# Kernel optimization log

Hardware: AMD Instinct MI355X
Metric: run time of the kernel (lower is better)

Reference implementation:

```python
import jax, jax.numpy as jnp
import numpy as np

B, S, T, E, H, F = 2, 2048, 2048, 1024, 16, 4096
HD = E // H
EPS = 1e-5


def setup_inputs() -> dict:
    key = jax.random.key(0)
    ks = jax.random.split(key, 16)
    def w(k, shape):
        return (jax.random.normal(k, shape, jnp.float32) * 0.02)
    d = {
        "x": jax.random.normal(ks[0], (B, S, E), jnp.float32),
        "enc": jax.random.normal(ks[1], (B, T, E), jnp.float32),
    }
    for i, n in enumerate(["sa_q", "sa_k", "sa_v", "sa_o", "ca_q", "ca_k", "ca_v", "ca_o"]):
        d[n + "w"] = w(ks[2 + i], (E, E))  # torch Linear: [out, in]
        d[n + "b"] = jnp.zeros((E,), jnp.float32)
    d["w1"] = w(ks[10], (F, E)); d["b1"] = jnp.zeros((F,), jnp.float32)
    d["w2"] = w(ks[11], (E, F)); d["b2"] = jnp.zeros((E,), jnp.float32)
    for n in ["ln1", "ln2", "ln3"]:
        d[n + "_g"] = jnp.ones((E,), jnp.float32)
        d[n + "_b"] = jnp.zeros((E,), jnp.float32)
    return d


def _layernorm(x, g, b):
    m = jnp.mean(x, axis=-1, keepdims=True)
    v = jnp.mean((x - m) ** 2, axis=-1, keepdims=True)
    return (x - m) / jnp.sqrt(v + EPS) * g + b


def _heads(x, w, b):
    bsz, sl, _ = x.shape
    y = x @ w.T + b
    return y.reshape(bsz, sl, H, HD).transpose(0, 2, 1, 3)  # [B,H,S,hd]


def _mha(xq, xkv, qw, qb, kw, kb, vw, vb, ow, ob, causal):
    q = _heads(xq, qw, qb)
    k = _heads(xkv, kw, kb)
    v = _heads(xkv, vw, vb)
    scores = jnp.einsum('bhsd,bhtd->bhst', q, k) / np.sqrt(HD).astype(np.float32)
    if causal:
        sl, tl = scores.shape[-2], scores.shape[-1]
        mask = jnp.tril(jnp.ones((sl, tl), bool))
        scores = jnp.where(mask, scores, -jnp.inf)
    a = jax.nn.softmax(scores, axis=-1)
    o = jnp.einsum('bhst,bhtd->bhsd', a, v)
    o = o.transpose(0, 2, 1, 3).reshape(xq.shape[0], xq.shape[1], E)
    return o @ ow.T + ob


def reference(x, enc,
              sa_qw, sa_qb, sa_kw, sa_kb, sa_vw, sa_vb, sa_ow, sa_ob,
              ca_qw, ca_qb, ca_kw, ca_kb, ca_vw, ca_vb, ca_ow, ca_ob,
              w1, b1, w2, b2,
              ln1_g, ln1_b, ln2_g, ln2_b, ln3_g, ln3_b):
    sa = _mha(x, x, sa_qw, sa_qb, sa_kw, sa_kb, sa_vw, sa_vb, sa_ow, sa_ob, True)
    x = _layernorm(x + sa, ln1_g, ln1_b)
    ca = _mha(x, enc, ca_qw, ca_qb, ca_kw, ca_kb, ca_vw, ca_vb, ca_ow, ca_ob, False)
    x = _layernorm(x + ca, ln2_g, ln2_b)
    ffn = jax.nn.relu(x @ w1.T + b1) @ w2.T + b2
    return _layernorm(x + ffn, ln3_g, ln3_b)
```

## Files before the change

kernel.cpp:

```cpp
#include <hip/hip_runtime.h>
#include <hip/hip_bf16.h>
#include <stdint.h>

typedef __attribute__((ext_vector_type(8))) short s16x8;
typedef __attribute__((ext_vector_type(4))) short s16x4;
typedef __attribute__((ext_vector_type(4))) float f32x4;

#define DEV static __device__ __forceinline__

DEV ushort f2bu(float f){
  unsigned u = __builtin_bit_cast(unsigned, f);
  return (ushort)((u + 0x7fffu + ((u >> 16) & 1u)) >> 16);
}
DEV ushort f2bn(float f){
  return __builtin_bit_cast(ushort, __float2bfloat16(f));
}

DEV void gload16(const void* g, void* l){
  __builtin_amdgcn_global_load_lds((const __attribute__((address_space(1))) void*)g,
                                   (__attribute__((address_space(3))) void*)l, 16, 0, 0);
}

#define SCALE_C 0.18033688f

struct ConvArgs {
  const float* src[17];
  void*        dst[17];
  int blk_end[17];
  int nel[17];
  unsigned f32mask;
};

__global__ void __launch_bounds__(256) k_conv(ConvArgs a){
  int bi = blockIdx.x, seg = 0;
  while (bi >= a.blk_end[seg]) seg++;
  int b0 = seg ? a.blk_end[seg-1] : 0;
  long off = (long)(bi - b0)*2048 + (long)threadIdx.x*8;
  if (off >= a.nel[seg]) return;
  const float* s = a.src[seg] + off;
  f32x4 v0 = *(const f32x4*)s;
  f32x4 v1 = *(const f32x4*)(s+4);
  if ((a.f32mask >> seg) & 1u){
    float* d = (float*)a.dst[seg] + off;
    *(f32x4*)d = v0; *(f32x4*)(d+4) = v1;
  } else {
    ushort* d = (ushort*)a.dst[seg] + off;
    s16x8 o;
#pragma unroll
    for (int j = 0; j < 4; j++){ o[j] = (short)f2bu(v0[j]); o[4+j] = (short)f2bu(v1[j]); }
    *(s16x8*)d = o;
  }
}

__global__ void __launch_bounds__(256) k_gemm(const ushort* __restrict__ A, const ushort* __restrict__ W,
    const float* __restrict__ bias, ushort* __restrict__ Cb,
    int M, int N, int K, int lda, int ldb, float scale)
{
  __shared__ __align__(16) ushort lsA[2][128*64];
  __shared__ __align__(16) ushort lsB[2][128*64];
  const int t = threadIdx.x, w = t >> 6, u = t & 63, lr = u & 15, lk = u >> 4;
  const int m0 = blockIdx.y * 128, n0 = blockIdx.x * 128;
  const int wm = w >> 1, wn = w & 1;
  const int rA = t >> 3, c8 = (t & 7) * 8;
  const ushort* Ap = A + (size_t)(m0 + rA) * lda + c8;
  const ushort* Wp = W + (size_t)(n0 + rA) * ldb + c8;
  f32x4 acc[4][4] = {};
  const int nk = K >> 6;

  auto stage = [&](int k0, int buf){
#pragma unroll
    for (int j = 0; j < 4; j++){
      gload16(Ap + (size_t)j*32*lda + k0, &lsA[buf][0] + j*2048 + w*512);
      gload16(Wp + (size_t)j*32*ldb + k0, &lsB[buf][0] + j*2048 + w*512);
    }
  };
  stage(0, 0);
  for (int tk = 0; tk < nk; ++tk){
    __syncthreads();
    if (tk + 1 < nk) stage((tk + 1) << 6, (tk + 1) & 1);
    const ushort* La = &lsA[tk & 1][0];
    const ushort* Lb = &lsB[tk & 1][0];
#pragma unroll
    for (int ks = 0; ks < 2; ks++){
      s16x8 af[4], bfr[4];
#pragma unroll
      for (int i = 0; i < 4; i++) af[i]  = *(const s16x8*)(La + (wm*64 + i*16 + lr)*64 + ks*32 + lk*8);
#pragma unroll
      for (int i = 0; i < 4; i++) bfr[i] = *(const s16x8*)(Lb + (wn*64 + i*16 + lr)*64 + ks*32 + lk*8);
#pragma unroll
      for (int mi = 0; mi < 4; mi++)
#pragma unroll
        for (int ni = 0; ni < 4; ni++)
          acc[mi][ni] = __builtin_amdgcn_mfma_f32_16x16x32_bf16(af[mi], bfr[ni], acc[mi][ni], 0, 0, 0);
    }
  }

#pragma unroll
  for (int mi = 0; mi < 4; mi++){
#pragma unroll
    for (int ni = 0; ni < 4; ni++){
      const int row = m0 + wm*64 + mi*16 + lk*4;
      const int col = n0 + wn*64 + ni*16 + lr;
      const float bv = bias[col];
#pragma unroll
      for (int i = 0; i < 4; i++){
        float v = (acc[mi][ni][i] + bv) * scale;
        Cb[(size_t)(row + i) * N + col] = f2bn(v);
      }
    }
  }
}

__global__ void __launch_bounds__(256) k_gemmS(const ushort* __restrict__ A, const ushort* __restrict__ W,
    const float* __restrict__ bias, float* __restrict__ Cf,
    int M, int N, int Kext, int lda, int ldb, long long sstride)
{
  __shared__ __align__(16) ushort lsA[2][128*64];
  __shared__ __align__(16) ushort lsB[2][128*64];
  const int t = threadIdx.x, w = t >> 6, u = t & 63, lr = u & 15, lk = u >> 4;
  const int m0 = blockIdx.y * 128, n0 = blockIdx.x * 128;
  const int s = blockIdx.z;
  const int wm = w >> 1, wn = w & 1;
  const int rA = t >> 3, c8 = (t & 7) * 8;
  const ushort* Ap = A + (size_t)(m0 + rA) * lda + (size_t)s * Kext + c8;
  const ushort* Wp = W + (size_t)(n0 + rA) * ldb + (size_t)s * Kext + c8;
  if (s){ bias = nullptr; Cf += sstride; }
  f32x4 acc[4][4] = {};
  const int nk = Kext >> 6;

  auto stage = [&](int k0, int buf){
#pragma unroll
    for (int j = 0; j < 4; j++){
      gload16(Ap + (size_t)j*32*lda + k0, &lsA[buf][0] + j*2048 + w*512);
      gload16(Wp + (size_t)j*32*ldb + k0, &lsB[buf][0] + j*2048 + w*512);
    }
  };
  stage(0, 0);
  for (int tk = 0; tk < nk; ++tk){
    __syncthreads();
    if (tk + 1 < nk) stage((tk + 1) << 6, (tk + 1) & 1);
    const ushort* La = &lsA[tk & 1][0];
    const ushort* Lb = &lsB[tk & 1][0];
#pragma unroll
    for (int ks = 0; ks < 2; ks++){
      s16x8 af[4], bfr[4];
#pragma unroll
      for (int i = 0; i < 4; i++) af[i]  = *(const s16x8*)(La + (wm*64 + i*16 + lr)*64 + ks*32 + lk*8);
#pragma unroll
      for (int i = 0; i < 4; i++) bfr[i] = *(const s16x8*)(Lb + (wn*64 + i*16 + lr)*64 + ks*32 + lk*8);
#pragma unroll
      for (int mi = 0; mi < 4; mi++)
#pragma unroll
        for (int ni = 0; ni < 4; ni++)
          acc[mi][ni] = __builtin_amdgcn_mfma_f32_16x16x32_bf16(af[mi], bfr[ni], acc[mi][ni], 0, 0, 0);
    }
  }

#pragma unroll
  for (int mi = 0; mi < 4; mi++){
#pragma unroll
    for (int ni = 0; ni < 4; ni++){
      const int row = m0 + wm*64 + mi*16 + lk*4;
      const int col = n0 + wn*64 + ni*16 + lr;
      const float bv = bias ? bias[col] : 0.f;
#pragma unroll
      for (int i = 0; i < 4; i++)
        Cf[(size_t)(row + i) * N + col] = acc[mi][ni][i] + bv;
    }
  }
}

template<int MODE>
__global__ void __launch_bounds__(512, 1) k_gemm256(const ushort* __restrict__ A, const ushort* __restrict__ W,
    const float* __restrict__ bias, ushort* __restrict__ Cb,
    int N, int Ktot, int lda, int ldb, int scaleLim, float scale)
{
  __shared__ __align__(16) ushort lsA[2][256*64];
  __shared__ __align__(16) ushort lsB[2][256*64];
  const int t = threadIdx.x, w = t >> 6, u = t & 63, lr = u & 15, lk = u >> 4;
  const int gx = gridDim.x;
  const int nwg = gx * gridDim.y;
  const int id = blockIdx.y * gx + blockIdx.x;
  const int swz = (id & 7) * (nwg >> 3) + (id >> 3);
  const int n0 = (swz % gx) * 256, m0 = (swz / gx) * 256;
  const int wm = w >> 2, wn = w & 3;
  const int nt = Ktot >> 6;

  const int r0 = w*8 + (u >> 3), cc = u & 7;
  const int csw = 8 * (cc ^ (r0 & 7));
  const ushort* Ap = A + (size_t)(m0 + r0) * lda + csw;
  const ushort* Wp = W + (size_t)(n0 + r0) * ldb + csw;

  f32x4 acc[8][4] = {};
  const int swl = lr & 7;
  s16x8 afr[4], bfr[4];

#pragma unroll
  for (int j = 0; j < 4; j++){
    gload16(Ap + (size_t)(64*j)*lda, &lsA[0][0] + w*512 + j*4096);
    gload16(Wp + (size_t)(64*j)*ldb, &lsB[0][0] + w*512 + j*4096);
  }
  asm volatile("s_waitcnt vmcnt(0)" ::: "memory");
  __builtin_amdgcn_s_barrier();

  for (int tk = 0; tk < nt; ++tk){
    const char* La = (const char*)&lsA[tk & 1][0];
    const char* Lb = (const char*)&lsB[tk & 1][0];
    ushort* dA = &lsA[(tk & 1) ^ 1][0] + w*512;
    ushort* dB = &lsB[(tk & 1) ^ 1][0] + w*512;
    const bool pf = (tk + 1 < nt);
    const size_t k1 = (size_t)(tk + 1) << 6;

#pragma unroll
    for (int i = 0; i < 4; i++)
      afr[i] = *(const s16x8*)(La + (wm*128 + i*16 + lr)*128 + ((lk ^ swl) * 16));
#pragma unroll
    for (int i = 0; i < 4; i++)
      bfr[i] = *(const s16x8*)(Lb + (wn*64 + i*16 + lr)*128 + ((lk ^ swl) * 16));
    if (pf){
      gload16(Ap + k1, dA);
      gload16(Wp + k1, dB);
      gload16(Ap + (size_t)64*lda + k1, dA + 4096);
      gload16(Wp + (size_t)64*ldb + k1, dB + 4096);
    }
    __builtin_amdgcn_s_barrier();
    asm volatile("s_waitcnt lgkmcnt(0)" ::: "memory");
    __builtin_amdgcn_s_setprio(1);
#pragma unroll
    for (int mi = 0; mi < 4; mi++)
#pragma unroll
      for (int ni = 0; ni < 4; ni++)
        acc[mi][ni] = __builtin_amdgcn_mfma_f32_16x16x32_bf16(afr[mi], bfr[ni], acc[mi][ni], 0, 0, 0);
    __builtin_amdgcn_s_setprio(0);
    __builtin_amdgcn_s_barrier();

#pragma unroll
    for (int i = 0; i < 4; i++)
      afr[i] = *(const s16x8*)(La + (wm*128 + 64 + i*16 + lr)*128 + ((lk ^ swl) * 16));
    if (pf){
      gload16(Ap + (size_t)128*lda + k1, dA + 8192);
      gload16(Wp + (size_t)128*ldb + k1, dB + 8192);
      gload16(Ap + (size_t)192*lda + k1, dA + 12288);
      gload16(Wp + (size_t)192*ldb + k1, dB + 12288);
    }
    __builtin_amdgcn_s_barrier();
    asm volatile("s_waitcnt lgkmcnt(0)" ::: "memory");
    __builtin_amdgcn_s_setprio(1);
#pragma unroll
    for (int mi = 0; mi < 4; mi++)
#pragma unroll
      for (int ni = 0; ni < 4; ni++)
        acc[4+mi][ni] = __builtin_amdgcn_mfma_f32_16x16x32_bf16(afr[mi], bfr[ni], acc[4+mi][ni], 0, 0, 0);
    __builtin_amdgcn_s_setprio(0);
    __builtin_amdgcn_s_barrier();

#pragma unroll
    for (int i = 0; i < 4; i++)
      afr[i] = *(const s16x8*)(La + (wm*128 + i*16 + lr)*128 + (((4 + lk) ^ swl) * 16));
#pragma unroll
    for (int i = 0; i < 4; i++)
      bfr[i] = *(const s16x8*)(Lb + (wn*64 + i*16 + lr)*128 + (((4 + lk) ^ swl) * 16));
    __builtin_amdgcn_s_barrier();
    asm volatile("s_waitcnt lgkmcnt(0)" ::: "memory");
    __builtin_amdgcn_s_setprio(1);
#pragma unroll
    for (int mi = 0; mi < 4; mi++)
#pragma unroll
      for (int ni = 0; ni < 4; ni++)
        acc[mi][ni] = __builtin_amdgcn_mfma_f32_16x16x32_bf16(afr[mi], bfr[ni], acc[mi][ni], 0, 0, 0);
    __builtin_amdgcn_s_setprio(0);
    __builtin_amdgcn_s_barrier();

#pragma unroll
    for (int i = 0; i < 4; i++)
      afr[i] = *(const s16x8*)(La + (wm*128 + 64 + i*16 + lr)*128 + (((4 + lk) ^ swl) * 16));
    __builtin_amdgcn_s_barrier();
    asm volatile("s_waitcnt lgkmcnt(0)" ::: "memory");
    __builtin_amdgcn_s_setprio(1);
#pragma unroll
    for (int mi = 0; mi < 4; mi++)
#pragma unroll
      for (int ni = 0; ni < 4; ni++)
        acc[4+mi][ni] = __builtin_amdgcn_mfma_f32_16x16x32_bf16(afr[mi], bfr[ni], acc[4+mi][ni], 0, 0, 0);
    __builtin_amdgcn_s_setprio(0);
    asm volatile("s_waitcnt vmcnt(0)" ::: "memory");
    __builtin_amdgcn_s_barrier();
  }

#pragma unroll
  for (int mi = 0; mi < 8; mi++){
#pragma unroll
    for (int ni = 0; ni < 4; ni++){
      const int row = m0 + wm*128 + mi*16 + lk*4;
      const int col = n0 + wn*64 + ni*16 + lr;
      const float bv = bias[col];
#pragma unroll
      for (int i = 0; i < 4; i++){
        float v = acc[mi][ni][i] + bv;
        if (MODE == 2) v = fmaxf(v, 0.f);
        if (MODE == 0 && col < scaleLim) v *= scale;
        Cb[(size_t)(row + i) * N + col] = f2bn(v);
      }
    }
  }
}

__global__ void __launch_bounds__(256) k_vt(const ushort* __restrict__ V, ushort* __restrict__ Vt,
                                            int stride, int S)
{
  __shared__ ushort tile[64][72];
  const int st = blockIdx.x*64, h = blockIdx.y, b = blockIdx.z;
  const int r = threadIdx.x >> 3, c8 = (threadIdx.x & 7)*8;
#pragma unroll
  for (int j = 0; j < 2; j++){
    int s = r + j*32;
    s16x8 v = *(const s16x8*)(V + (size_t)(b*S + st + s)*stride + h*64 + c8);
    *(s16x8*)&tile[s][c8] = v;
  }
  __syncthreads();
#pragma unroll
  for (int j = 0; j < 2; j++){
    int d = r + j*32;
    s16x8 o;
#pragma unroll
    for (int e = 0; e < 8; e++) o[e] = tile[c8+e][d];
    *(s16x8*)(Vt + ((size_t)((b*16 + h)*64 + d))*S + st + c8) = o;
  }
}

template<bool CAUSAL>
__global__ void __launch_bounds__(512, 4) k_attn(const ushort* __restrict__ Q, const ushort* __restrict__ Kg,
    const ushort* __restrict__ Vt, ushort* __restrict__ O, int sQ, int sK, int SQ, int SKV)
{
  __shared__ __align__(16) ushort Kl[2][128*64];
  __shared__ __align__(16) ushort Vl[2][64*128];
  __shared__ __align__(16) ushort Pl[8][16*64];
  const int t = threadIdx.x, w = t >> 6, u = t & 63, lr = u & 15, lk = u >> 4;
  const int hb = blockIdx.x;
  const int b = hb >> 4, h = hb & 15;
  const int krow = t >> 3, kcol = t & 7;
  const int vrow = t >> 4, vcol = t & 15;
  const size_t kvbase = (size_t)b * SKV;
  const size_t vtbase = (size_t)((b*16 + h)*64);
  char* Pc = (char*)&Pl[w][0];
  const int swzq = (lr & 7) << 4;

  auto stage = [&](int kt, int buf){
#pragma unroll
    for (int p = 0; p < 2; p++){
      int row = krow + p*64;
      gload16(Kg + (kvbase + kt*128 + row)*sK + h*64 + 8*(kcol ^ (row & 7)),
              &Kl[buf][0] + t*8 + p*4096);
      int d = vrow + p*32;
      gload16(Vt + (vtbase + d)*SKV + kt*128 + 8*(vcol ^ (d & 7)),
              &Vl[buf][0] + t*8 + p*4096);
    }
  };

  const int NREP = CAUSAL ? 2 : 1;
#pragma unroll 1
  for (int rep = 0; rep < NREP; rep++){
    const int qt = CAUSAL ? (rep ? (int)blockIdx.y : (int)(2*gridDim.y - 1 - blockIdx.y))
                          : (int)blockIdx.y;
    const int q0 = qt * 128;

    const ushort* qp = Q + (size_t)(b*SQ + q0 + w*16 + lr) * sQ + h*64 + lk*8;
    s16x8 qf0 = *(const s16x8*)qp;
    s16x8 qf1 = *(const s16x8*)(qp + 32);

    f32x4 oacc[4] = {};
    f32x4 lacc = {};
    const int nkt = CAUSAL ? (qt + 1) : (SKV >> 7);

    stage(0, 0);
    __syncthreads();

    for (int kt = 0; kt < nkt; kt++){
      const int buf = kt & 1;
      if (kt + 1 < nkt) stage(kt + 1, buf ^ 1);
      char* Kc = (char*)&Kl[buf][0];
      char* Vc = (char*)&Vl[buf][0];

      f32x4 sacc[8] = {};
      __builtin_amdgcn_s_setprio(1);
#pragma unroll
      for (int ks = 0; ks < 2; ks++){
        s16x8 qf = ks ? qf1 : qf0;
#pragma unroll
        for (int ni = 0; ni < 8; ni++){
          int key = ni*16 + lr;
          s16x8 kf = *(const s16x8*)(Kc + key*128 + ((ks*64 + lk*16) ^ ((key & 7) << 4)));
          sacc[ni] = __builtin_amdgcn_mfma_f32_16x16x32_bf16(kf, qf, sacc[ni], 0, 0, 0);
        }
      }
      __builtin_amdgcn_s_setprio(0);
      if (CAUSAL && kt == qt){
#pragma unroll
        for (int ni = 0; ni < 8; ni++)
#pragma unroll
          for (int i = 0; i < 4; i++)
            if (16*ni + lk*4 + i > w*16 + lr) sacc[ni][i] = -1e30f;
      }

#pragma unroll
      for (int ni = 0; ni < 8; ni++){
#pragma unroll
        for (int i = 0; i < 4; i++) sacc[ni][i] = __builtin_exp2f(sacc[ni][i]);
        lacc += sacc[ni];
      }

#pragma unroll
      for (int hf = 0; hf < 2; hf++){
#pragma unroll
        for (int ni = 0; ni < 4; ni++){
          s16x4 pk;
#pragma unroll
          for (int i = 0; i < 4; i++) pk[i] = (short)f2bn(sacc[hf*4 + ni][i]);
          *(s16x4*)(Pc + lr*128 + ((32*ni + 8*lk) ^ swzq)) = pk;
        }
        __builtin_amdgcn_s_setprio(1);
#pragma unroll
        for (int ks = 0; ks < 2; ks++){
          s16x8 pf = *(const s16x8*)(Pc + lr*128 + ((ks*64 + lk*16) ^ swzq));
#pragma unroll
          for (int ni = 0; ni < 4; ni++){
            int d = ni*16 + lr;
            s16x8 vf = *(const s16x8*)(Vc + d*256 + ((hf*128 + ks*64 + lk*16) ^ ((d & 7) << 4)));
            oacc[ni] = __builtin_amdgcn_mfma_f32_16x16x32_bf16(pf, vf, oacc[ni], 0, 0, 0);
          }
        }
        __builtin_amdgcn_s_setprio(0);
      }
      __syncthreads();
    }

    float lrun = lacc[0] + lacc[1] + lacc[2] + lacc[3];
    lrun += __shfl_xor(lrun, 16);
    lrun += __shfl_xor(lrun, 32);
    float il = 1.f / lrun;
    float invl[4];
#pragma unroll
    for (int i = 0; i < 4; i++) invl[i] = __shfl(il, lk*4 + i);
#pragma unroll
    for (int ni = 0; ni < 4; ni++)
#pragma unroll
      for (int i = 0; i < 4; i++)
        O[(size_t)(b*SQ + q0 + w*16 + lk*4 + i)*1024 + h*64 + ni*16 + lr] = f2bn(oacc[ni][i] * invl[i]);
  }
}

template<bool WB16>
__global__ void __launch_bounds__(256) k_ln(const float* __restrict__ R, const float* __restrict__ P,
    const float* __restrict__ P2, const float* __restrict__ G, const float* __restrict__ Bv,
    float* __restrict__ Of, ushort* __restrict__ Ob)
{
  const int row = blockIdx.x, t = threadIdx.x, w = t >> 6, u = t & 63;
  const size_t base = (size_t)row * 1024 + t * 4;
  f32x4 r = *(const f32x4*)(R + base);
  f32x4 p = *(const f32x4*)(P + base);
  f32x4 v = r + p;
  if (P2){ f32x4 p2 = *(const f32x4*)(P2 + base); v += p2; }
  float s = 0.f, q = 0.f;
#pragma unroll
  for (int j = 0; j < 4; j++){ s += v[j]; q += v[j]*v[j]; }
#pragma unroll
  for (int md = 1; md < 64; md <<= 1){ s += __shfl_xor(s, md); q += __shfl_xor(q, md); }
  __shared__ float ps[4], pq[4];
  if (u == 0){ ps[w] = s; pq[w] = q; }
  __syncthreads();
  s = ps[0] + ps[1] + ps[2] + ps[3];
  q = pq[0] + pq[1] + pq[2] + pq[3];
  const float mean = s * (1.f/1024.f);
  const float var  = q * (1.f/1024.f) - mean*mean;
  const float rstd = rsqrtf(var + 1e-5f);
  f32x4 g4 = *(const f32x4*)(G  + t*4);
  f32x4 b4 = *(const f32x4*)(Bv + t*4);
  f32x4 o;
#pragma unroll
  for (int j = 0; j < 4; j++) o[j] = (v[j] - mean) * rstd * g4[j] + b4[j];
  *(f32x4*)(Of + base) = o;
  if (WB16){
    s16x4 ob;
#pragma unroll
    for (int j = 0; j < 4; j++) ob[j] = (short)f2bn(o[j]);
    *(s16x4*)(Ob + base) = ob;
  }
}

extern "C" void kernel_launch(void* const* d_in, const int* in_sizes, int n_in,
                              void* d_out, int out_size, void* d_ws, size_t ws_size,
                              hipStream_t stream)
{
  const float* x   = (const float*)d_in[0];
  const float* enc = (const float*)d_in[1];
  const float* aw[8]; const float* ab[8];
  for (int i = 0; i < 8; i++){ aw[i] = (const float*)d_in[2 + 2*i]; ab[i] = (const float*)d_in[3 + 2*i]; }
  const float* w1 = (const float*)d_in[18]; const float* b1 = (const float*)d_in[19];
  const float* w2 = (const float*)d_in[20]; const float* b2 = (const float*)d_in[21];
  const float* lg[3] = {(const float*)d_in[22], (const float*)d_in[24], (const float*)d_in[26]};
  const float* lb[3] = {(const float*)d_in[23], (const float*)d_in[25], (const float*)d_in[27]};
  float* out = (float*)d_out;

  const size_t MB = 1024ull * 1024ull;
  if (ws_size < 129 * MB) return;
  char* ws = (char*)d_ws;
  ushort* wqkv = (ushort*)(ws + 0*MB);
  ushort* wcq  = (ushort*)(ws + 6*MB);
  ushort* wkv  = (ushort*)(ws + 8*MB);
  ushort* wo1w = (ushort*)(ws + 12*MB);
  ushort* wo2w = (ushort*)(ws + 14*MB);
  ushort* w1b  = (ushort*)(ws + 16*MB);
  ushort* w2b  = (ushort*)(ws + 24*MB);
  ushort* xb   = (ushort*)(ws + 32*MB);
  ushort* encb = (ushort*)(ws + 40*MB);
  ushort* attb = (ushort*)(ws + 48*MB);
  float*  proj = (float*)(ws + 56*MB);
  float*  x1f  = (float*)(ws + 72*MB);
  ushort* xab  = (ushort*)(ws + 88*MB);
  ushort* QKVb    = (ushort*)(ws + 96*MB);
  ushort* Vt1     = (ushort*)(ws + 120*MB);
  ushort* crossQb = (ushort*)(ws + 96*MB);
  ushort* encKVb  = (ushort*)(ws + 104*MB);
  ushort* Vt2     = (ushort*)(ws + 120*MB);
  ushort* hb      = (ushort*)(ws + 96*MB);
  float*  pWO     = (float*)(ws + 96*MB);
  float*  pFF     = (float*)(ws + 32*MB);
  float*  bqkv = (float*)(ws + 128*MB);
  float*  bkv  = (float*)(ws + 128*MB + 16384);

  const long long ssWO  = ((long long)(96 - 56) * (long long)MB) / 4;
  const long long ssFFN = ((long long)(32 - 56) * (long long)MB) / 4;

  ConvArgs ca;
  const float* srcs[17] = { x, enc, aw[0], aw[1], aw[2], aw[3], aw[4], aw[5], aw[6], aw[7],
                            w1, w2, ab[0], ab[1], ab[2], ab[5], ab[6] };
  void* dsts[17] = { xb, encb, wqkv, wqkv + 1048576, wqkv + 2097152, wo1w, wcq, wkv, wkv + 1048576, wo2w,
                     w1b, w2b, bqkv, bqkv + 1024, bqkv + 2048, bkv, bkv + 1024 };
  int nels[17] = { 4194304, 4194304, 1048576, 1048576, 1048576, 1048576, 1048576, 1048576, 1048576, 1048576,
                   4194304, 4194304, 1024, 1024, 1024, 1024, 1024 };
  int acc_blk = 0;
  for (int i = 0; i < 17; i++){
    ca.src[i] = srcs[i]; ca.dst[i] = dsts[i]; ca.nel[i] = nels[i];
    acc_blk += (nels[i] + 2047) / 2048;
    ca.blk_end[i] = acc_blk;
  }
  ca.f32mask = 0x1F000u;
  k_conv<<<acc_blk, 256, 0, stream>>>(ca);

  k_gemm256<0><<<dim3(12,16), 512, 0, stream>>>(xb, wqkv, bqkv, QKVb, 3072, 1024, 1024, 1024, 1024, SCALE_C);
  k_vt<<<dim3(32,16,2), 256, 0, stream>>>(QKVb + 2048, Vt1, 3072, 2048);
  k_attn<true><<<dim3(32,8), 512, 0, stream>>>(QKVb, QKVb + 1024, Vt1, attb, 3072, 3072, 2048, 2048);
  k_gemmS<<<dim3(8,32,2), 256, 0, stream>>>(attb, wo1w, ab[3], proj, 4096, 1024, 512, 1024, 1024, ssWO);
  k_ln<true><<<4096, 256, 0, stream>>>(x, proj, pWO, lg[0], lb[0], x1f, xab);

  k_gemm<<<dim3(8,32), 256, 0, stream>>>(xab, wcq, ab[4], crossQb, 4096, 1024, 1024, 1024, 1024, SCALE_C);
  k_gemm256<0><<<dim3(8,16), 512, 0, stream>>>(encb, wkv, bkv, encKVb, 2048, 1024, 1024, 1024, 0, 1.f);
  k_vt<<<dim3(32,16,2), 256, 0, stream>>>(encKVb + 1024, Vt2, 2048, 2048);
  k_attn<false><<<dim3(32,16), 512, 0, stream>>>(crossQb, encKVb, Vt2, attb, 1024, 2048, 2048, 2048);
  k_gemmS<<<dim3(8,32,2), 256, 0, stream>>>(attb, wo2w, ab[7], proj, 4096, 1024, 512, 1024, 1024, ssWO);
  k_ln<true><<<4096, 256, 0, stream>>>(x1f, proj, pWO, lg[1], lb[1], x1f, xab);

  k_gemm256<2><<<dim3(16,16), 512, 0, stream>>>(xab, w1b, b1, hb, 4096, 1024, 1024, 1024, 0, 1.f);
  k_gemmS<<<dim3(8,32,2), 256, 0, stream>>>(hb, w2b, b2, proj, 4096, 1024, 2048, 4096, 4096, ssFFN);
  k_ln<false><<<4096, 256, 0, stream>>>(x1f, proj, pFF, lg[2], lb[2], out, nullptr);
}
```

Baseline: 394.7 us.

## Triple-buffer attention KV tiles at 64 keys with vmcnt-based waits

Shrinks the attention key/value tile from 128 to 64 keys and triple-buffers it in LDS, prefetching two tiles ahead. Explicit s_waitcnt vmcnt plus raw s_barrier replace __syncthreads so global-to-LDS loads stay in flight across iterations. The causal mask now covers the two diagonal 64-key tiles, and the occupancy hint in launch_bounds is dropped. Smaller tiles mean twice as many barriers per row and less MFMA work between syncs, and the extra clamped reload on the last tiles adds some redundant traffic.

```diff
diff --git a/kernel.cpp b/kernel.cpp
--- a/kernel.cpp
+++ b/kernel.cpp
@@ -329,32 +329,24 @@
 }
 
 template<bool CAUSAL>
-__global__ void __launch_bounds__(512, 4) k_attn(const ushort* __restrict__ Q, const ushort* __restrict__ Kg,
+__global__ void __launch_bounds__(512) k_attn(const ushort* __restrict__ Q, const ushort* __restrict__ Kg,
     const ushort* __restrict__ Vt, ushort* __restrict__ O, int sQ, int sK, int SQ, int SKV)
 {
-  __shared__ __align__(16) ushort Kl[2][128*64];
-  __shared__ __align__(16) ushort Vl[2][64*128];
+  __shared__ __align__(16) ushort Kl[3][64*64];
+  __shared__ __align__(16) ushort Vl[3][64*64];
   __shared__ __align__(16) ushort Pl[8][16*64];
   const int t = threadIdx.x, w = t >> 6, u = t & 63, lr = u & 15, lk = u >> 4;
   const int hb = blockIdx.x;
   const int b = hb >> 4, h = hb & 15;
-  const int krow = t >> 3, kcol = t & 7;
-  const int vrow = t >> 4, vcol = t & 15;
+  const int srow = t >> 3, scol = t & 7;
   const size_t kvbase = (size_t)b * SKV;
   const size_t vtbase = (size_t)((b*16 + h)*64);
   char* Pc = (char*)&Pl[w][0];
   const int swzq = (lr & 7) << 4;
 
   auto stage = [&](int kt, int buf){
-#pragma unroll
-    for (int p = 0; p < 2; p++){
-      int row = krow + p*64;
-      gload16(Kg + (kvbase + kt*128 + row)*sK + h*64 + 8*(kcol ^ (row & 7)),
-              &Kl[buf][0] + t*8 + p*4096);
-      int d = vrow + p*32;
-      gload16(Vt + (vtbase + d)*SKV + kt*128 + 8*(vcol ^ (d & 7)),
-              &Vl[buf][0] + t*8 + p*4096);
-    }
+    gload16(Kg + (kvbase + kt*64 + srow)*sK + h*64 + 8*(scol ^ (srow & 7)), &Kl[buf][0] + w*512);
+    gload16(Vt + (vtbase + srow)*SKV + kt*64 + 8*(scol ^ (srow & 7)), &Vl[buf][0] + w*512);
   };
 
   const int NREP = CAUSAL ? 2 : 1;
@@ -370,68 +362,73 @@
 
     f32x4 oacc[4] = {};
     f32x4 lacc = {};
-    const int nkt = CAUSAL ? (qt + 1) : (SKV >> 7);
-
+    const int nkt = CAUSAL ? (2*qt + 2) : (SKV >> 6);
+
+    asm volatile("s_waitcnt vmcnt(0)" ::: "memory");
     stage(0, 0);
-    __syncthreads();
-
+    stage(1, 1);
+
+#pragma unroll 1
     for (int kt = 0; kt < nkt; kt++){
-      const int buf = kt & 1;
-      if (kt + 1 < nkt) stage(kt + 1, buf ^ 1);
-      char* Kc = (char*)&Kl[buf][0];
-      char* Vc = (char*)&Vl[buf][0];
-
-      f32x4 sacc[8] = {};
+      const int bi = kt % 3;
+      const int tn = (kt + 2 < nkt) ? (kt + 2) : (nkt - 1);
+      stage(tn, (kt + 2) % 3);
+      asm volatile("s_waitcnt vmcnt(4)" ::: "memory");
+      __builtin_amdgcn_s_barrier();
+
+      char* Kc = (char*)&Kl[bi][0];
+      char* Vc = (char*)&Vl[bi][0];
+
+      f32x4 sacc[4] = {};
       __builtin_amdgcn_s_setprio(1);
 #pragma unroll
       for (int ks = 0; ks < 2; ks++){
         s16x8 qf = ks ? qf1 : qf0;
 #pragma unroll
-        for (int ni = 0; ni < 8; ni++){
+        for (int ni = 0; ni < 4; ni++){
           int key = ni*16 + lr;
           s16x8 kf = *(const s16x8*)(Kc + key*128 + ((ks*64 + lk*16) ^ ((key & 7) << 4)));
           sacc[ni] = __builtin_amdgcn_mfma_f32_16x16x32_bf16(kf, qf, sacc[ni], 0, 0, 0);
         }
       }
       __builtin_amdgcn_s_setprio(0);
-      if (CAUSAL && kt == qt){
-#pragma unroll
-        for (int ni = 0; ni < 8; ni++)
+      if (CAUSAL && kt >= 2*qt){
+        const int koff = kt*64 - q0;
+#pragma unroll
+        for (int ni = 0; ni < 4; ni++)
 #pragma unroll
           for (int i = 0; i < 4; i++)
-            if (16*ni + lk*4 + i > w*16 + lr) sacc[ni][i] = -1e30f;
-      }
-
-#pragma unroll
-      for (int ni = 0; ni < 8; ni++){
+            if (koff + 16*ni + lk*4 + i > w*16 + lr) sacc[ni][i] = -1e30f;
+      }
+
+#pragma unroll
+      for (int ni = 0; ni < 4; ni++){
 #pragma unroll
         for (int i = 0; i < 4; i++) sacc[ni][i] = __builtin_exp2f(sacc[ni][i]);
         lacc += sacc[ni];
       }
 
 #pragma unroll
-      for (int hf = 0; hf < 2; hf++){
+      for (int ni = 0; ni < 4; ni++){
+        s16x4 pk;
+#pragma unroll
+        for (int i = 0; i < 4; i++) pk[i] = (short)f2bn(sacc[ni][i]);
+        *(s16x4*)(Pc + lr*128 + ((32*ni + 8*lk) ^ swzq)) = pk;
+      }
+
+      __builtin_amdgcn_s_setprio(1);
+#pragma unroll
+      for (int ks = 0; ks < 2; ks++){
+        s16x8 pf = *(const s16x8*)(Pc + lr*128 + ((ks*64 + lk*16) ^ swzq));
 #pragma unroll
         for (int ni = 0; ni < 4; ni++){
-          s16x4 pk;
-#pragma unroll
-          for (int i = 0; i < 4; i++) pk[i] = (short)f2bn(sacc[hf*4 + ni][i]);
-          *(s16x4*)(Pc + lr*128 + ((32*ni + 8*lk) ^ swzq)) = pk;
+          int d = ni*16 + lr;
+          s16x8 vf = *(const s16x8*)(Vc + d*128 + ((ks*64 + lk*16) ^ ((d & 7) << 4)));
+          oacc[ni] = __builtin_amdgcn_mfma_f32_16x16x32_bf16(pf, vf, oacc[ni], 0, 0, 0);
         }
-        __builtin_amdgcn_s_setprio(1);
-#pragma unroll
-        for (int ks = 0; ks < 2; ks++){
-          s16x8 pf = *(const s16x8*)(Pc + lr*128 + ((ks*64 + lk*16) ^ swzq));
-#pragma unroll
-          for (int ni = 0; ni < 4; ni++){
-            int d = ni*16 + lr;
-            s16x8 vf = *(const s16x8*)(Vc + d*256 + ((hf*128 + ks*64 + lk*16) ^ ((d & 7) << 4)));
-            oacc[ni] = __builtin_amdgcn_mfma_f32_16x16x32_bf16(pf, vf, oacc[ni], 0, 0, 0);
-          }
-        }
-        __builtin_amdgcn_s_setprio(0);
-      }
-      __syncthreads();
+      }
+      __builtin_amdgcn_s_setprio(0);
+      __builtin_amdgcn_s_barrier();
     }
 
     float lrun = lacc[0] + lacc[1] + lacc[2] + lacc[3];
```

New measurement: 399.8 us. About the same (+1.3%).

## Rewrite attention with 32x32 MFMA tiles and register-resident P operand

Applied to the files above, without the earlier changes.

The attention kernel moves from 16x16x32 MFMAs with 8 waves of 16 query rows to 32x32x16 MFMAs with 4 waves of 32 query rows, and KV tiles shrink from 128 to 64 keys. The probability matrix no longer round-trips through LDS: it is packed with v_cvt_pk_bf16_f32 and rearranged across half-waves with shuffles to form the A operand of the PV MFMA. Causal masking is also finer-grained at 64-key granularity. This removes LDS write/read traffic for P and cuts LDS per block. In exchange it adds more loop iterations and barriers, uses more registers per wave, and leaves fewer waves per block to hide latency.

```diff
diff --git a/kernel.cpp b/kernel.cpp
--- a/kernel.cpp
+++ b/kernel.cpp
@@ -2,9 +2,11 @@
 #include <hip/hip_bf16.h>
 #include <stdint.h>
 
-typedef __attribute__((ext_vector_type(8))) short s16x8;
-typedef __attribute__((ext_vector_type(4))) short s16x4;
-typedef __attribute__((ext_vector_type(4))) float f32x4;
+typedef __attribute__((ext_vector_type(8)))  short s16x8;
+typedef __attribute__((ext_vector_type(4)))  short s16x4;
+typedef __attribute__((ext_vector_type(4)))  float f32x4;
+typedef __attribute__((ext_vector_type(16))) float f32x16;
+typedef __attribute__((ext_vector_type(4)))  int   s32x4;
 
 #define DEV static __device__ __forceinline__
 
@@ -14,6 +16,11 @@
 }
 DEV ushort f2bn(float f){
   return __builtin_bit_cast(ushort, __float2bfloat16(f));
+}
+DEV unsigned cvtpk(float lo, float hi){
+  unsigned d;
+  asm("v_cvt_pk_bf16_f32 %0, %1, %2" : "=v"(d) : "v"(lo), "v"(hi));
+  return d;
 }
 
 DEV void gload16(const void* g, void* l){
@@ -329,31 +336,27 @@
 }
 
 template<bool CAUSAL>
-__global__ void __launch_bounds__(512, 4) k_attn(const ushort* __restrict__ Q, const ushort* __restrict__ Kg,
+__global__ void __launch_bounds__(256) k_attn(const ushort* __restrict__ Q, const ushort* __restrict__ Kg,
     const ushort* __restrict__ Vt, ushort* __restrict__ O, int sQ, int sK, int SQ, int SKV)
 {
-  __shared__ __align__(16) ushort Kl[2][128*64];
-  __shared__ __align__(16) ushort Vl[2][64*128];
-  __shared__ __align__(16) ushort Pl[8][16*64];
-  const int t = threadIdx.x, w = t >> 6, u = t & 63, lr = u & 15, lk = u >> 4;
+  __shared__ __align__(16) ushort Kl[2][64*64];
+  __shared__ __align__(16) ushort Vl[2][64*64];
+  const int t = threadIdx.x, l = t & 63, wq = t >> 6;
+  const int hi = l >> 5, q32 = l & 31;
   const int hb = blockIdx.x;
   const int b = hb >> 4, h = hb & 15;
-  const int krow = t >> 3, kcol = t & 7;
-  const int vrow = t >> 4, vcol = t & 15;
+  const int srow = t >> 3, scol = t & 7;
   const size_t kvbase = (size_t)b * SKV;
   const size_t vtbase = (size_t)((b*16 + h)*64);
-  char* Pc = (char*)&Pl[w][0];
-  const int swzq = (lr & 7) << 4;
 
   auto stage = [&](int kt, int buf){
 #pragma unroll
     for (int p = 0; p < 2; p++){
-      int row = krow + p*64;
-      gload16(Kg + (kvbase + kt*128 + row)*sK + h*64 + 8*(kcol ^ (row & 7)),
-              &Kl[buf][0] + t*8 + p*4096);
-      int d = vrow + p*32;
-      gload16(Vt + (vtbase + d)*SKV + kt*128 + 8*(vcol ^ (d & 7)),
-              &Vl[buf][0] + t*8 + p*4096);
+      int row = srow + p*32;
+      gload16(Kg + (kvbase + kt*64 + row)*sK + h*64 + 8*(scol ^ (row & 7)),
+              &Kl[buf][0] + p*2048 + t*8);
+      gload16(Vt + (vtbase + row)*SKV + kt*64 + 8*(scol ^ (row & 7)),
+              &Vl[buf][0] + p*2048 + t*8);
     }
   };
 
@@ -363,89 +366,102 @@
     const int qt = CAUSAL ? (rep ? (int)blockIdx.y : (int)(2*gridDim.y - 1 - blockIdx.y))
                           : (int)blockIdx.y;
     const int q0 = qt * 128;
-
-    const ushort* qp = Q + (size_t)(b*SQ + q0 + w*16 + lr) * sQ + h*64 + lk*8;
-    s16x8 qf0 = *(const s16x8*)qp;
-    s16x8 qf1 = *(const s16x8*)(qp + 32);
-
-    f32x4 oacc[4] = {};
-    f32x4 lacc = {};
-    const int nkt = CAUSAL ? (qt + 1) : (SKV >> 7);
+    const int qg = q0 + wq*32 + q32;
+
+    const ushort* qp = Q + (size_t)(b*SQ + qg) * sQ + h*64 + hi*8;
+    s16x8 qf[4];
+#pragma unroll
+    for (int st2 = 0; st2 < 4; st2++) qf[st2] = *(const s16x8*)(qp + st2*16);
+
+    f32x16 oacc[2] = {};
+    float lsum = 0.f;
+    const int nkt = CAUSAL ? (2*qt + 2) : (SKV >> 6);
 
     stage(0, 0);
     __syncthreads();
 
+#pragma unroll 1
     for (int kt = 0; kt < nkt; kt++){
       const int buf = kt & 1;
       if (kt + 1 < nkt) stage(kt + 1, buf ^ 1);
-      char* Kc = (char*)&Kl[buf][0];
-      char* Vc = (char*)&Vl[buf][0];
-
-      f32x4 sacc[8] = {};
+      const char* Kc = (const char*)&Kl[buf][0];
+      const char* Vc = (const char*)&Vl[buf][0];
+
+      f32x16 sacc[2] = {};
       __builtin_amdgcn_s_setprio(1);
 #pragma unroll
-      for (int ks = 0; ks < 2; ks++){
-        s16x8 qf = ks ? qf1 : qf0;
-#pragma unroll
-        for (int ni = 0; ni < 8; ni++){
-          int key = ni*16 + lr;
-          s16x8 kf = *(const s16x8*)(Kc + key*128 + ((ks*64 + lk*16) ^ ((key & 7) << 4)));
-          sacc[ni] = __builtin_amdgcn_mfma_f32_16x16x32_bf16(kf, qf, sacc[ni], 0, 0, 0);
+      for (int mg = 0; mg < 2; mg++){
+        const int krow = 32*mg + q32;
+#pragma unroll
+        for (int st2 = 0; st2 < 4; st2++){
+          s16x8 kf = *(const s16x8*)(Kc + krow*128 + (((st2*2 + hi) ^ (krow & 7)) * 16));
+          sacc[mg] = __builtin_amdgcn_mfma_f32_32x32x16_bf16(kf, qf[st2], sacc[mg], 0, 0, 0);
         }
       }
       __builtin_amdgcn_s_setprio(0);
-      if (CAUSAL && kt == qt){
-#pragma unroll
-        for (int ni = 0; ni < 8; ni++)
-#pragma unroll
-          for (int i = 0; i < 4; i++)
-            if (16*ni + lk*4 + i > w*16 + lr) sacc[ni][i] = -1e30f;
+
+      if (CAUSAL && kt >= 2*qt){
+#pragma unroll
+        for (int mg = 0; mg < 2; mg++)
+#pragma unroll
+          for (int r = 0; r < 16; r++){
+            int key = kt*64 + 32*mg + (r & 3) + 8*(r >> 2) + 4*hi;
+            if (key > qg) sacc[mg][r] = -1e30f;
+          }
       }
 
 #pragma unroll
-      for (int ni = 0; ni < 8; ni++){
-#pragma unroll
-        for (int i = 0; i < 4; i++) sacc[ni][i] = __builtin_exp2f(sacc[ni][i]);
-        lacc += sacc[ni];
-      }
-
-#pragma unroll
-      for (int hf = 0; hf < 2; hf++){
-#pragma unroll
-        for (int ni = 0; ni < 4; ni++){
-          s16x4 pk;
-#pragma unroll
-          for (int i = 0; i < 4; i++) pk[i] = (short)f2bn(sacc[hf*4 + ni][i]);
-          *(s16x4*)(Pc + lr*128 + ((32*ni + 8*lk) ^ swzq)) = pk;
+      for (int mg = 0; mg < 2; mg++)
+#pragma unroll
+        for (int r = 0; r < 16; r++){
+          float p = __builtin_exp2f(sacc[mg][r]);
+          sacc[mg][r] = p; lsum += p;
         }
-        __builtin_amdgcn_s_setprio(1);
+
+      __builtin_amdgcn_s_setprio(1);
+#pragma unroll
+      for (int mg = 0; mg < 2; mg++){
+        unsigned dw[8];
+#pragma unroll
+        for (int j = 0; j < 8; j++) dw[j] = cvtpk(sacc[mg][2*j], sacc[mg][2*j+1]);
 #pragma unroll
         for (int ks = 0; ks < 2; ks++){
-          s16x8 pf = *(const s16x8*)(Pc + lr*128 + ((ks*64 + lk*16) ^ swzq));
-#pragma unroll
-          for (int ni = 0; ni < 4; ni++){
-            int d = ni*16 + lr;
-            s16x8 vf = *(const s16x8*)(Vc + d*256 + ((hf*128 + ks*64 + lk*16) ^ ((d & 7) << 4)));
-            oacc[ni] = __builtin_amdgcn_mfma_f32_16x16x32_bf16(pf, vf, oacc[ni], 0, 0, 0);
+          unsigned j0 = dw[ks*4+0], j1 = dw[ks*4+1], j2 = dw[ks*4+2], j3 = dw[ks*4+3];
+          unsigned x0 = __shfl_xor(j0, 32), x1 = __shfl_xor(j1, 32);
+          unsigned x2 = __shfl_xor(j2, 32), x3 = __shfl_xor(j3, 32);
+          s32x4 av;
+          av[0] = (int)(hi ? x2 : j0);
+          av[1] = (int)(hi ? x3 : j1);
+          av[2] = (int)(hi ? j2 : x0);
+          av[3] = (int)(hi ? j3 : x1);
+          s16x8 af = __builtin_bit_cast(s16x8, av);
+          const int kchunk = mg*4 + ks*2 + hi;
+#pragma unroll
+          for (int dh = 0; dh < 2; dh++){
+            const int drow = q32 + 32*dh;
+            s16x8 vf = *(const s16x8*)(Vc + drow*128 + ((kchunk ^ (drow & 7)) * 16));
+            oacc[dh] = __builtin_amdgcn_mfma_f32_32x32x16_bf16(af, vf, oacc[dh], 0, 0, 0);
           }
         }
-        __builtin_amdgcn_s_setprio(0);
       }
+      __builtin_amdgcn_s_setprio(0);
       __syncthreads();
     }
 
-    float lrun = lacc[0] + lacc[1] + lacc[2] + lacc[3];
-    lrun += __shfl_xor(lrun, 16);
-    lrun += __shfl_xor(lrun, 32);
-    float il = 1.f / lrun;
-    float invl[4];
-#pragma unroll
-    for (int i = 0; i < 4; i++) invl[i] = __shfl(il, lk*4 + i);
-#pragma unroll
-    for (int ni = 0; ni < 4; ni++)
-#pragma unroll
-      for (int i = 0; i < 4; i++)
-        O[(size_t)(b*SQ + q0 + w*16 + lk*4 + i)*1024 + h*64 + ni*16 + lr] = f2bn(oacc[ni][i] * invl[i]);
+    lsum += __shfl_xor(lsum, 32);
+    float il = 1.f / lsum;
+    float invl[16];
+#pragma unroll
+    for (int r = 0; r < 16; r++)
+      invl[r] = __shfl(il, (r & 3) + 8*(r >> 2) + 4*hi);
+
+#pragma unroll
+    for (int dh = 0; dh < 2; dh++)
+#pragma unroll
+      for (int r = 0; r < 16; r++){
+        int qrow = q0 + wq*32 + (r & 3) + 8*(r >> 2) + 4*hi;
+        O[(size_t)(b*SQ + qrow)*1024 + h*64 + q32 + 32*dh] = f2bn(oacc[dh][r] * invl[r]);
+      }
   }
 }
 
@@ -549,14 +565,14 @@
 
   k_gemm256<0><<<dim3(12,16), 512, 0, stream>>>(xb, wqkv, bqkv, QKVb, 3072, 1024, 1024, 1024, 1024, SCALE_C);
   k_vt<<<dim3(32,16,2), 256, 0, stream>>>(QKVb + 2048, Vt1, 3072, 2048);
-  k_attn<true><<<dim3(32,8), 512, 0, stream>>>(QKVb, QKVb + 1024, Vt1, attb, 3072, 3072, 2048, 2048);
+  k_attn<true><<<dim3(32,8), 256, 0, stream>>>(QKVb, QKVb + 1024, Vt1, attb, 3072, 3072, 2048, 2048);
   k_gemmS<<<dim3(8,32,2), 256, 0, stream>>>(attb, wo1w, ab[3], proj, 4096, 1024, 512, 1024, 1024, ssWO);
   k_ln<true><<<4096, 256, 0, stream>>>(x, proj, pWO, lg[0], lb[0], x1f, xab);
 
   k_gemm<<<dim3(8,32), 256, 0, stream>>>(xab, wcq, ab[4], crossQb, 4096, 1024, 1024, 1024, 1024, SCALE_C);
   k_gemm256<0><<<dim3(8,16), 512, 0, stream>>>(encb, wkv, bkv, encKVb, 2048, 1024, 1024, 1024, 0, 1.f);
   k_vt<<<dim3(32,16,2), 256, 0, stream>>>(encKVb + 1024, Vt2, 2048, 2048);
-  k_attn<false><<<dim3(32,16), 512, 0, stream>>>(crossQb, encKVb, Vt2, attb, 1024, 2048, 2048, 2048);
+  k_attn<false><<<dim3(32,16), 256, 0, stream>>>(crossQb, encKVb, Vt2, attb, 1024, 2048, 2048, 2048);
   k_gemmS<<<dim3(8,32,2), 256, 0, stream>>>(attb, wo2w, ab[7], proj, 4096, 1024, 512, 1024, 1024, ssWO);
   k_ln<true><<<4096, 256, 0, stream>>>(x1f, proj, pWO, lg[1], lb[1], x1f, xab);
 
```

New measurement: 418.4 us. +6.0%, slower.
